# Kernel tuning notes

Measured on AMD Instinct MI355X. Metric: run time of the kernel, lower is better.

## Reference

```python
import jax, jax.numpy as jnp
import numpy as np

EPS = 1e-5
GROUPS = 32


def group_norm(x, gamma, beta):
    b, c, h, w = x.shape
    xg = x.reshape(b, GROUPS, c // GROUPS, h, w)
    mu = xg.mean(axis=(2, 3, 4), keepdims=True)
    var = xg.var(axis=(2, 3, 4), keepdims=True)
    xn = ((xg - mu) * jax.lax.rsqrt(var + EPS)).reshape(b, c, h, w)
    return xn * gamma[None, :, None, None] + beta[None, :, None, None]


def setup_inputs() -> dict:
    key = jax.random.key(0)
    ks = jax.random.split(key, 4)
    b, c, h, w = 4, 512, 64, 64
    x = jax.random.normal(ks[0], (b, c, h, w), dtype=jnp.float32)
    gn_w = jnp.ones((c,), jnp.float32)
    gn_b = jnp.zeros((c,), jnp.float32)
    qkv_w = jax.random.normal(ks[1], (3 * c, c), dtype=jnp.float32) * (c ** -0.5)
    qkv_b = jnp.zeros((3 * c,), jnp.float32)
    out_w = jax.random.normal(ks[2], (c, c), dtype=jnp.float32) * (c ** -0.5)
    out_b = jnp.zeros((c,), jnp.float32)
    return {"x": x, "gn_w": gn_w, "gn_b": gn_b, "qkv_w": qkv_w,
            "qkv_b": qkv_b, "out_w": out_w, "out_b": out_b}


def reference(x, gn_w, gn_b, qkv_w, qkv_b, out_w, out_b):
    b, c, hh, ww = x.shape
    n = hh * ww
    h = group_norm(x, gn_w, gn_b)
    # 1x1 conv == per-pixel matmul over channels
    qkv = jnp.einsum('bchw,oc->bohw', h, qkv_w) + qkv_b[None, :, None, None]
    q, k, v = jnp.split(qkv, 3, axis=1)
    q = q.transpose(0, 2, 3, 1).reshape(b, n, c)   # (b, n, c)
    k = k.reshape(b, c, n)                          # (b, c, n)
    v = v.transpose(0, 2, 3, 1).reshape(b, n, c)   # (b, n, c)
    attn = jax.nn.softmax(jnp.einsum('bnc,bcm->bnm', q, k) * (c ** -0.5), axis=-1)
    out = jnp.einsum('bnm,bmc->bnc', attn, v)
    out = out.reshape(b, hh, ww, c).transpose(0, 3, 1, 2)
    out = jnp.einsum('bchw,oc->bohw', out, out_w) + out_b[None, :, None, None]
    return out + x
```

## Files before the change

### kernel.cpp

```cpp
#include <hip/hip_runtime.h>
#include <cmath>

#define NB 4
#define NC 512
#define NN 4096
#define ATTN_SCALE 0.04419417382415922f

typedef __bf16 bf16x8 __attribute__((ext_vector_type(8)));
typedef float floatx4 __attribute__((ext_vector_type(4)));

__device__ __forceinline__ unsigned short f2bf(float f) {
    union { float f; unsigned int u; } v; v.f = f;
    return (unsigned short)((v.u + 0x7fffu + ((v.u >> 16) & 1u)) >> 16);
}
__device__ __forceinline__ unsigned short f2bf_trunc(float f) {
    union { float f; unsigned int u; } v; v.f = f;
    return (unsigned short)(v.u >> 16);
}

__device__ __forceinline__ void gload_lds16(const unsigned short* gp, unsigned short* lp) {
    __builtin_amdgcn_global_load_lds(
        (const __attribute__((address_space(1))) void*)gp,
        (__attribute__((address_space(3))) void*)lp, 16, 0, 0);
}

template<int N> __device__ __forceinline__ void wait_vmcnt() {
    if constexpr (N == 0) asm volatile("s_waitcnt vmcnt(0)" ::: "memory");
    else if constexpr (N == 3) asm volatile("s_waitcnt vmcnt(3)" ::: "memory");
    else if constexpr (N == 4) asm volatile("s_waitcnt vmcnt(4)" ::: "memory");
    else if constexpr (N == 6) asm volatile("s_waitcnt vmcnt(6)" ::: "memory");
}

__global__ __launch_bounds__(256) void gn_partial_kernel(
    const float* __restrict__ x, float* __restrict__ part)
{
    int blk = blockIdx.x;
    int bg = blk >> 3, sub = blk & 7;
    const float4* xv = (const float4*)(x + (size_t)bg * 16 * NN + (size_t)sub * 8192);
    float s1 = 0.f, s2 = 0.f;
#pragma unroll
    for (int i = 0; i < 8; ++i) {
        float4 v = xv[threadIdx.x + i * 256];
        s1 += v.x + v.y + v.z + v.w;
        s2 += v.x * v.x + v.y * v.y + v.z * v.z + v.w * v.w;
    }
#pragma unroll
    for (int off = 32; off; off >>= 1) {
        s1 += __shfl_xor(s1, off, 64);
        s2 += __shfl_xor(s2, off, 64);
    }
    __shared__ float r1[4], r2[4];
    int lane = threadIdx.x & 63, w = threadIdx.x >> 6;
    if (lane == 0) { r1[w] = s1; r2[w] = s2; }
    __syncthreads();
    if (threadIdx.x == 0) {
        part[blk * 2]     = r1[0] + r1[1] + r1[2] + r1[3];
        part[blk * 2 + 1] = r2[0] + r2[1] + r2[2] + r2[3];
    }
}

__global__ __launch_bounds__(128) void gn_final_kernel(
    const float* __restrict__ part, const float* __restrict__ gw,
    const float* __restrict__ gb, float* __restrict__ ss)
{
    int tg = threadIdx.x;
    int b = tg >> 5, g = tg & 31;
    float s1 = 0.f, s2 = 0.f;
#pragma unroll
    for (int s = 0; s < 8; ++s) {
        s1 += part[(tg * 8 + s) * 2];
        s2 += part[(tg * 8 + s) * 2 + 1];
    }
    float mean = s1 * (1.0f / 65536.0f);
    float var  = s2 * (1.0f / 65536.0f) - mean * mean;
    float rstd = rsqrtf(var + 1e-5f);
#pragma unroll
    for (int i = 0; i < 16; ++i) {
        int c = g * 16 + i;
        float sc = rstd * gw[c];
        ss[b * NC + c] = sc;
        ss[2048 + b * NC + c] = gb[c] - mean * sc;
    }
}

__global__ __launch_bounds__(256) void wconv_kernel(
    const float* __restrict__ qkv_w, const float* __restrict__ out_w,
    unsigned short* __restrict__ wq, unsigned short* __restrict__ wo)
{
    int i = blockIdx.x * 256 + threadIdx.x;
    const int NQ = 1536 * 512;
    if (i < NQ) wq[i] = f2bf(qkv_w[i]);
    else        wo[i - NQ] = f2bf(out_w[i - NQ]);
}

__global__ __launch_bounds__(256) void htnorm_kernel(
    const float* __restrict__ x, const float* __restrict__ ss,
    unsigned short* __restrict__ ht)
{
    int b = blockIdx.z;
    int c0 = blockIdx.y * 32, n0 = blockIdx.x * 32;
    __shared__ float T[32][33];
    int tx = threadIdx.x & 31, ty = threadIdx.x >> 5;
    const float* xb = x + ((size_t)b * NC + c0) * NN;
    const float* sc = ss + b * NC + c0;
    const float* sh = ss + 2048 + b * NC + c0;
#pragma unroll
    for (int i = 0; i < 4; ++i) {
        int c = ty + i * 8;
        T[c][tx] = xb[(size_t)c * NN + n0 + tx] * sc[c] + sh[c];
    }
    __syncthreads();
    unsigned short* hb = ht + ((size_t)b * NN + n0) * NC + c0;
#pragma unroll
    for (int i = 0; i < 4; ++i) {
        int n = ty + i * 8;
        hb[(size_t)n * NC + tx] = f2bf(T[tx][n]);
    }
}

template<int MODE, int BM, int BN, int KD, int NBUF, int MINB>
__global__ __launch_bounds__(256, MINB) void mfma_gemm(
    const unsigned short* __restrict__ Abase,
    const unsigned short* __restrict__ Bbase,
    const float* __restrict__ e0, const float* __restrict__ e1,
    float* __restrict__ outf,
    unsigned short* __restrict__ ob0, unsigned short* __restrict__ ob1)
{
    constexpr int NT = KD / 32;
    constexpr int FI = BM / 32;
    constexpr int FJ = BN / 32;
    constexpr int LPS = BM / 64 + BN / 64;
    constexpr int DEPTH = NBUF - 1;
    const size_t bnc = (size_t)NN * NC;
    const size_t bss = (size_t)NN * NN;

    int z, m0, n0;
    if constexpr (MODE == 2) {
        const int id = blockIdx.x;
        const int xcd = id & 7, j = id >> 3;
        const int mi = xcd * 8 + (j & 7);
        z = mi >> 4; m0 = (mi & 15) * BM; n0 = (j >> 3) * BN;
    } else {
        z = blockIdx.z; m0 = blockIdx.y * BM; n0 = blockIdx.x * BN;
    }

    const unsigned short* A;
    const unsigned short* B;
    if constexpr (MODE == 0)      { A = Abase + (size_t)z * bnc; B = Bbase; }
    else if constexpr (MODE == 1) { A = Abase; B = Bbase + (size_t)z * bnc; }
    else if constexpr (MODE == 2) { A = Abase + (size_t)z * bnc; B = Bbase + (size_t)z * bnc; }
    else                          { A = Abase; B = Bbase + (size_t)z * bnc; }

    __shared__ __attribute__((aligned(16))) unsigned short As[NBUF][BM * 32];
    __shared__ __attribute__((aligned(16))) unsigned short Bs[NBUF][BN * 32];

    const int t = threadIdx.x;
    const int lane = t & 63;
    const int w = t >> 6;
    const int wr = w >> 1, wc = w & 1;

    const int sr = w * 16 + (lane >> 2);
    const int scs = ((lane & 3) ^ ((lane >> 3) & 3)) * 8;
    const int lds_elem = w * 512;
    const int kslot = lane >> 4;

    floatx4 acc[FI][FJ] = {};

    auto stage = [&](int buf, int tile) {
        const int k0 = tile * 32;
#pragma unroll
        for (int s = 0; s < BM / 64; ++s)
            gload_lds16(A + (size_t)(m0 + s * 64 + sr) * KD + k0 + scs,
                        &As[buf][s * 2048 + lds_elem]);
#pragma unroll
        for (int s = 0; s < BN / 64; ++s)
            gload_lds16(B + (size_t)(n0 + s * 64 + sr) * KD + k0 + scs,
                        &Bs[buf][s * 2048 + lds_elem]);
    };

    auto compute = [&](int buf) {
        bf16x8 af[FI], bfr[FJ];
#pragma unroll
        for (int i = 0; i < FI; ++i) {
            const int ra = wr * (BM / 2) + i * 16 + (lane & 15);
            af[i] = *(const bf16x8*)(&As[buf][ra * 32 + ((kslot ^ ((ra >> 1) & 3)) * 8)]);
        }
#pragma unroll
        for (int j = 0; j < FJ; ++j) {
            const int rb = wc * (BN / 2) + j * 16 + (lane & 15);
            bfr[j] = *(const bf16x8*)(&Bs[buf][rb * 32 + ((kslot ^ ((rb >> 1) & 3)) * 8)]);
        }
#pragma unroll
        for (int i = 0; i < FI; ++i)
#pragma unroll
            for (int j = 0; j < FJ; ++j)
                acc[i][j] = __builtin_amdgcn_mfma_f32_16x16x32_bf16(
                    af[i], bfr[j], acc[i][j], 0, 0, 0);
    };

#pragma unroll
    for (int d = 0; d < DEPTH; ++d) stage(d, d);
    wait_vmcnt<(DEPTH - 1) * LPS>();
    __builtin_amdgcn_s_barrier();

#pragma unroll
    for (int kt = 0; kt < NT - DEPTH; ++kt) {
        stage((kt + DEPTH) % NBUF, kt + DEPTH);
        compute(kt % NBUF);
        asm volatile("s_waitcnt lgkmcnt(0)" ::: "memory");
        wait_vmcnt<(DEPTH - 1) * LPS>();
        __builtin_amdgcn_s_barrier();
    }

    compute((NT - 2) % NBUF);
    asm volatile("s_waitcnt lgkmcnt(0)" ::: "memory");
    wait_vmcnt<0>();
    __builtin_amdgcn_s_barrier();
    compute((NT - 1) % NBUF);

    const int fr = lane >> 4;
    const int fc = lane & 15;

    if constexpr (MODE == 2) {
        float rs[FI][4];
#pragma unroll
        for (int i = 0; i < FI; ++i)
#pragma unroll
            for (int r = 0; r < 4; ++r) rs[i][r] = 0.f;
#pragma unroll
        for (int i = 0; i < FI; ++i) {
#pragma unroll
            for (int j = 0; j < FJ; ++j) {
                int n = n0 + wc * (BN / 2) + j * 16 + fc;
                int mbase = m0 + wr * (BM / 2) + i * 16 + fr * 4;
#pragma unroll
                for (int r = 0; r < 4; ++r) {
                    float e = __expf(acc[i][j][r]);
                    ob0[(size_t)z * bss + (size_t)(mbase + r) * NN + n] = f2bf_trunc(e);
                    rs[i][r] += e;
                }
            }
        }
#pragma unroll
        for (int i = 0; i < FI; ++i) {
#pragma unroll
            for (int r = 0; r < 4; ++r) {
                float v = rs[i][r];
                v += __shfl_xor(v, 1, 16);
                v += __shfl_xor(v, 2, 16);
                v += __shfl_xor(v, 4, 16);
                v += __shfl_xor(v, 8, 16);
                if (fc == 0) {
                    int m = m0 + wr * (BM / 2) + i * 16 + fr * 4 + r;
                    atomicAdd(&outf[z * NN + m], v);
                }
            }
        }
        return;
    }

#pragma unroll
    for (int i = 0; i < FI; ++i) {
#pragma unroll
        for (int j = 0; j < FJ; ++j) {
            int n = n0 + wc * (BN / 2) + j * 16 + fc;
            int mbase = m0 + wr * (BM / 2) + i * 16 + fr * 4;
#pragma unroll
            for (int r = 0; r < 4; ++r) {
                int m = mbase + r;
                float val = acc[i][j][r];
                if constexpr (MODE == 0) {
                    val += e0[n];
                    if (n < 512) ob0[((size_t)z * NN + m) * NC + n] = f2bf(val * ATTN_SCALE);
                    else         ob1[((size_t)z * NN + m) * NC + (n - 512)] = f2bf(val);
                } else if constexpr (MODE == 1) {
                    val += e0[1024 + m];
                    ob0[((size_t)z * NC + m) * NN + n] = f2bf(val);
                } else {
                    size_t idx = ((size_t)z * NC + m) * NN + n;
                    outf[idx] = val + e0[m] + e1[idx];
                }
            }
        }
    }
}

__global__ __launch_bounds__(256, 2) void pv_gemm(
    const unsigned short* __restrict__ Abase,
    const unsigned short* __restrict__ Bbase,
    const float* __restrict__ L,
    unsigned short* __restrict__ Ob)
{
    const int id = blockIdx.x;
    const int xcd = id & 7;
    const int j0 = id >> 3;
    const int ct = j0 & 3;
    const int p = (j0 >> 2) * 8 + xcd;
    const int ptile = p & 31, z = p >> 5;

    const size_t bss = (size_t)NN * NN, bnc = (size_t)NN * NC;
    const unsigned short* A = Abase + (size_t)z * bss;
    const unsigned short* B = Bbase + (size_t)z * bnc;
    const int m0 = ptile * 128;
    const int n0 = ct * 128;

    __shared__ __attribute__((aligned(16))) unsigned short As[2][128 * 64];
    __shared__ __attribute__((aligned(16))) unsigned short Bs[2][128 * 64];

    const int t = threadIdx.x;
    const int lane = t & 63;
    const int w = t >> 6;
    const int wr = w >> 1, wc = w & 1;

    const int sr = w * 8 + (lane >> 3);
    const int scs = ((lane & 7) ^ (lane >> 3)) * 8;
    const int lds_elem = w * 512;

    floatx4 acc[4][4] = {};

    auto stage = [&](int buf, int k0) {
#pragma unroll
        for (int s = 0; s < 4; ++s)
            gload_lds16(A + (size_t)(m0 + s * 32 + sr) * NN + k0 + scs,
                        &As[buf][s * 2048 + lds_elem]);
#pragma unroll
        for (int s = 0; s < 4; ++s)
            gload_lds16(B + (size_t)(n0 + s * 32 + sr) * NN + k0 + scs,
                        &Bs[buf][s * 2048 + lds_elem]);
    };

    auto compute = [&](int buf) {
#pragma unroll
        for (int kk = 0; kk < 2; ++kk) {
            bf16x8 af[4], bfr[4];
#pragma unroll
            for (int i = 0; i < 4; ++i) {
                const int ra = wr * 64 + i * 16 + (lane & 15);
                af[i] = *(const bf16x8*)(&As[buf][ra * 64 +
                        (((kk * 4 + (lane >> 4)) ^ (ra & 7)) * 8)]);
            }
#pragma unroll
            for (int jf = 0; jf < 4; ++jf) {
                const int rb = wc * 64 + jf * 16 + (lane & 15);
                bfr[jf] = *(const bf16x8*)(&Bs[buf][rb * 64 +
                        (((kk * 4 + (lane >> 4)) ^ (rb & 7)) * 8)]);
            }
#pragma unroll
            for (int i = 0; i < 4; ++i)
#pragma unroll
                for (int jf = 0; jf < 4; ++jf)
                    acc[i][jf] = __builtin_amdgcn_mfma_f32_16x16x32_bf16(
                        af[i], bfr[jf], acc[i][jf], 0, 0, 0);
        }
    };

    stage(0, 0);
    asm volatile("s_waitcnt vmcnt(0)" ::: "memory");
    __builtin_amdgcn_s_barrier();
    for (int kc = 0; kc < 63; ++kc) {
        stage((kc + 1) & 1, (kc + 1) * 64);
        compute(kc & 1);
        asm volatile("s_waitcnt lgkmcnt(0)" ::: "memory");
        asm volatile("s_waitcnt vmcnt(0)" ::: "memory");
        __builtin_amdgcn_s_barrier();
    }
    compute(1);

    const int fr = lane >> 4;
    const int fc = lane & 15;
#pragma unroll
    for (int i = 0; i < 4; ++i) {
#pragma unroll
        for (int r = 0; r < 4; ++r) {
            int m = m0 + wr * 64 + i * 16 + fr * 4 + r;
            float linv = 1.0f / L[z * NN + m];
#pragma unroll
            for (int jf = 0; jf < 4; ++jf) {
                int n = n0 + wc * 64 + jf * 16 + fc;
                Ob[(size_t)z * bnc + (size_t)m * NC + n] = f2bf(acc[i][jf][r] * linv);
            }
        }
    }
}

extern "C" void kernel_launch(void* const* d_in, const int* in_sizes, int n_in,
                              void* d_out, int out_size, void* d_ws, size_t ws_size,
                              hipStream_t stream)
{
    const float* x     = (const float*)d_in[0];
    const float* gn_w  = (const float*)d_in[1];
    const float* gn_b  = (const float*)d_in[2];
    const float* qkv_w = (const float*)d_in[3];
    const float* qkv_b = (const float*)d_in[4];
    const float* out_w = (const float*)d_in[5];
    const float* out_b = (const float*)d_in[6];
    float* out = (float*)d_out;

    const size_t bnc = (size_t)NN * NC;
    char* w = (char*)d_ws;
    float* ss   = (float*)w;                 w += 16384;
    float* part = (float*)w;                 w += 8192;
    float* Lsum = (float*)w;                 w += (size_t)NB * NN * 4;
    unsigned short* wq = (unsigned short*)w; w += (size_t)1536 * 512 * 2;
    unsigned short* wo = (unsigned short*)w; w += (size_t)512 * 512 * 2;
    unsigned short* qt = (unsigned short*)w; w += NB * bnc * 2;
    unsigned short* kt = (unsigned short*)w; w += NB * bnc * 2;
    unsigned short* vt = (unsigned short*)w; w += NB * bnc * 2;
    unsigned short* SP = (unsigned short*)w; w += (size_t)NB * NN * NN * 2;
    unsigned short* ht = SP;
    unsigned short* Ob = qt;

    hipMemsetAsync(Lsum, 0, (size_t)NB * NN * sizeof(float), stream);

    gn_partial_kernel<<<1024, 256, 0, stream>>>(x, part);
    gn_final_kernel<<<1, 128, 0, stream>>>(part, gn_w, gn_b, ss);
    wconv_kernel<<<(1536 * 512 + 512 * 512) / 256, 256, 0, stream>>>(qkv_w, out_w, wq, wo);
    htnorm_kernel<<<dim3(NN / 32, NC / 32, NB), 256, 0, stream>>>(x, ss, ht);

    mfma_gemm<0, 128, 128, 512, 3, 3><<<dim3(1024 / 128, NN / 128, NB), 256, 0, stream>>>(
        ht, wq, qkv_b, nullptr, nullptr, qt, kt);
    mfma_gemm<1, 64, 128, 512, 3, 4><<<dim3(NN / 128, 512 / 64, NB), 256, 0, stream>>>(
        wq + (size_t)1024 * 512, ht, qkv_b, nullptr, nullptr, vt, nullptr);

    mfma_gemm<2, 256, 128, 512, 3, 2><<<dim3(2048), 256, 0, stream>>>(
        qt, kt, nullptr, nullptr, Lsum, SP, nullptr);
    pv_gemm<<<dim3(512), 256, 0, stream>>>(SP, vt, Lsum, Ob);

    mfma_gemm<4, 64, 128, 512, 3, 4><<<dim3(NN / 128, 512 / 64, NB), 256, 0, stream>>>(
        wo, Ob, out_b, x, out, nullptr, nullptr);
}
```

Before: 356.2 us.

## Double-buffer register fragments in mfma_gemm main loop with MFMA priority boost

Restructures the GEMM main loop so LDS fragment reads for the next K-tile are issued into a second register set while MFMAs run on the current one (ping-pong fragments, loop unrolled by two). MFMA bursts are wrapped in s_setprio to favour matrix issue, and the vmcnt wait moves ahead of the LDS reads. It also lowers the occupancy hint for the QKV GEMM from 3 to 2 blocks. The extra fragment registers raise register pressure and can cut occupancy, and the loop assumes NT is even.

Result: no change. 353.0 us (-0.9%).

```diff
diff --git a/kernel.cpp b/kernel.cpp
--- a/kernel.cpp
+++ b/kernel.cpp
@@ -118,7 +118,7 @@
     }
 }
 
-template<int MODE, int BM, int BN, int KD, int NBUF, int MINB>
+template<int MODE, int BM, int BN, int KD, int MINB>
 __global__ __launch_bounds__(256, MINB) void mfma_gemm(
     const unsigned short* __restrict__ Abase,
     const unsigned short* __restrict__ Bbase,
@@ -130,7 +130,6 @@
     constexpr int FI = BM / 32;
     constexpr int FJ = BN / 32;
     constexpr int LPS = BM / 64 + BN / 64;
-    constexpr int DEPTH = NBUF - 1;
     const size_t bnc = (size_t)NN * NC;
     const size_t bss = (size_t)NN * NN;
 
@@ -151,8 +150,8 @@
     else if constexpr (MODE == 2) { A = Abase + (size_t)z * bnc; B = Bbase + (size_t)z * bnc; }
     else                          { A = Abase; B = Bbase + (size_t)z * bnc; }
 
-    __shared__ __attribute__((aligned(16))) unsigned short As[NBUF][BM * 32];
-    __shared__ __attribute__((aligned(16))) unsigned short Bs[NBUF][BN * 32];
+    __shared__ __attribute__((aligned(16))) unsigned short As[3][BM * 32];
+    __shared__ __attribute__((aligned(16))) unsigned short Bs[3][BN * 32];
 
     const int t = threadIdx.x;
     const int lane = t & 63;
@@ -178,8 +177,7 @@
                         &Bs[buf][s * 2048 + lds_elem]);
     };
 
-    auto compute = [&](int buf) {
-        bf16x8 af[FI], bfr[FJ];
+    auto ds_frags = [&](int buf, bf16x8* af, bf16x8* bfr) {
 #pragma unroll
         for (int i = 0; i < FI; ++i) {
             const int ra = wr * (BM / 2) + i * 16 + (lane & 15);
@@ -190,33 +188,50 @@
             const int rb = wc * (BN / 2) + j * 16 + (lane & 15);
             bfr[j] = *(const bf16x8*)(&Bs[buf][rb * 32 + ((kslot ^ ((rb >> 1) & 3)) * 8)]);
         }
+    };
+
+    auto mfma_all = [&](const bf16x8* af, const bf16x8* bfr) {
+        __builtin_amdgcn_s_setprio(1);
 #pragma unroll
         for (int i = 0; i < FI; ++i)
 #pragma unroll
             for (int j = 0; j < FJ; ++j)
                 acc[i][j] = __builtin_amdgcn_mfma_f32_16x16x32_bf16(
                     af[i], bfr[j], acc[i][j], 0, 0, 0);
+        __builtin_amdgcn_s_setprio(0);
     };
 
-#pragma unroll
-    for (int d = 0; d < DEPTH; ++d) stage(d, d);
-    wait_vmcnt<(DEPTH - 1) * LPS>();
+    bf16x8 afA[FI], bfA[FJ], afB[FI], bfB[FJ];
+
+    stage(0, 0);
+    stage(1, 1);
+    wait_vmcnt<LPS>();
     __builtin_amdgcn_s_barrier();
-
-#pragma unroll
-    for (int kt = 0; kt < NT - DEPTH; ++kt) {
-        stage((kt + DEPTH) % NBUF, kt + DEPTH);
-        compute(kt % NBUF);
+    ds_frags(0, afA, bfA);
+
+#pragma unroll
+    for (int kp = 0; kp < (NT - 2) / 2; ++kp) {
+        const int kt = kp * 2;
+        stage((kt + 2) % 3, kt + 2);
+        wait_vmcnt<LPS>();
+        ds_frags((kt + 1) % 3, afB, bfB);
+        mfma_all(afA, bfA);
         asm volatile("s_waitcnt lgkmcnt(0)" ::: "memory");
-        wait_vmcnt<(DEPTH - 1) * LPS>();
         __builtin_amdgcn_s_barrier();
-    }
-
-    compute((NT - 2) % NBUF);
+
+        stage((kt + 3) % 3, kt + 3);
+        wait_vmcnt<LPS>();
+        ds_frags((kt + 2) % 3, afA, bfA);
+        mfma_all(afB, bfB);
+        asm volatile("s_waitcnt lgkmcnt(0)" ::: "memory");
+        __builtin_amdgcn_s_barrier();
+    }
+
+    wait_vmcnt<0>();
+    ds_frags((NT - 1) % 3, afB, bfB);
+    mfma_all(afA, bfA);
     asm volatile("s_waitcnt lgkmcnt(0)" ::: "memory");
-    wait_vmcnt<0>();
-    __builtin_amdgcn_s_barrier();
-    compute((NT - 1) % NBUF);
+    mfma_all(afB, bfB);
 
     const int fr = lane >> 4;
     const int fc = lane & 15;
@@ -417,15 +432,15 @@
     wconv_kernel<<<(1536 * 512 + 512 * 512) / 256, 256, 0, stream>>>(qkv_w, out_w, wq, wo);
     htnorm_kernel<<<dim3(NN / 32, NC / 32, NB), 256, 0, stream>>>(x, ss, ht);
 
-    mfma_gemm<0, 128, 128, 512, 3, 3><<<dim3(1024 / 128, NN / 128, NB), 256, 0, stream>>>(
+    mfma_gemm<0, 128, 128, 512, 2><<<dim3(1024 / 128, NN / 128, NB), 256, 0, stream>>>(
         ht, wq, qkv_b, nullptr, nullptr, qt, kt);
-    mfma_gemm<1, 64, 128, 512, 3, 4><<<dim3(NN / 128, 512 / 64, NB), 256, 0, stream>>>(
+    mfma_gemm<1, 64, 128, 512, 4><<<dim3(NN / 128, 512 / 64, NB), 256, 0, stream>>>(
         wq + (size_t)1024 * 512, ht, qkv_b, nullptr, nullptr, vt, nullptr);
 
-    mfma_gemm<2, 256, 128, 512, 3, 2><<<dim3(2048), 256, 0, stream>>>(
+    mfma_gemm<2, 256, 128, 512, 2><<<dim3(2048), 256, 0, stream>>>(
         qt, kt, nullptr, nullptr, Lsum, SP, nullptr);
     pv_gemm<<<dim3(512), 256, 0, stream>>>(SP, vt, Lsum, Ob);
 
-    mfma_gemm<4, 64, 128, 512, 3, 4><<<dim3(NN / 128, 512 / 64, NB), 256, 0, stream>>>(
+    mfma_gemm<4, 64, 128, 512, 4><<<dim3(NN / 128, 512 / 64, NB), 256, 0, stream>>>(
         wo, Ob, out_b, x, out, nullptr, nullptr);
 }
```
